# Kernel tuning notes

Measured on AMD Instinct MI355X. Metric: run time of the kernel, lower is better.

## Reference

```python
import jax, jax.numpy as jnp
import numpy as np

# Static config (matches init_kwargs)
T_Q, H_Q, W_Q = 8, 16, 16
T_K, H_K, W_K = 8, 16, 16
HEADS, QDIM = 8, 64


def _rel_dist(q_len, k_len):
    q_ratio = round(max(k_len / q_len, 1.0))
    k_ratio = round(max(q_len / k_len, 1.0))
    d = jnp.arange(q_len)[:, None] * q_ratio - jnp.arange(k_len)[None, :] * k_ratio
    return d + (k_len - 1) * k_ratio  # [q_len, k_len] int indices


def setup_inputs() -> dict:
    key = jax.random.key(0)
    k1, k2, k3, k4, k5 = jax.random.split(key, 5)
    B = 2
    q_tok = T_Q * H_Q * W_Q
    k_tok = T_K * H_K * W_K
    return {
        "query": jax.random.normal(k1, (B, HEADS, q_tok, QDIM), dtype=jnp.float32),
        "scores": jax.random.normal(k2, (B, HEADS, q_tok, k_tok), dtype=jnp.float32),
        "height_emb": jax.random.normal(k3, (2 * (max(H_Q, H_K) - 1) + 1, QDIM), dtype=jnp.float32),
        "width_emb": jax.random.normal(k4, (2 * (max(W_Q, W_K) - 1) + 1, QDIM), dtype=jnp.float32),
        "time_emb": jax.random.normal(k5, (2 * (max(T_Q, T_K) - 1) + 1, QDIM), dtype=jnp.float32),
    }


def reference(query, scores, height_emb, width_emb, time_emb):
    B = query.shape[0]
    # Relative-distance index tables (static)
    dist_h = _rel_dist(H_Q, H_K)  # [H_Q, H_K]
    dist_w = _rel_dist(W_Q, W_K)  # [W_Q, W_K]
    dist_t = _rel_dist(T_Q, T_K)  # [T_Q, T_K]
    Rh = height_emb[dist_h]  # [H_Q, H_K, C]
    Rw = width_emb[dist_w]   # [W_Q, W_K, C]
    Rt = time_emb[dist_t]    # [T_Q, T_K, C]
    q = query.reshape(B, HEADS, T_Q, H_Q, W_Q, QDIM)
    rel_h = jnp.einsum('bNthwc,hkc->bNthwk', q, Rh)  # k = key height
    rel_w = jnp.einsum('bNthwc,wkc->bNthwk', q, Rw)  # k = key width
    rel_t = jnp.einsum('bNthwc,tkc->bNthwk', q, Rt)  # k = key time
    s = scores.reshape(B, HEADS, T_Q, H_Q, W_Q, T_K, H_K, W_K)
    s = (s
         + rel_h[:, :, :, :, :, None, :, None]
         + rel_w[:, :, :, :, :, None, None, :]
         + rel_t[:, :, :, :, :, :, None, None])
    return s.reshape(B, HEADS, T_Q * H_Q * W_Q, T_K * H_K * W_K)
```

## Files before the change

### kernel.cpp

```cpp
#include <hip/hip_runtime.h>

#define T_Q 8
#define H_Q 16
#define W_Q 16
#define HEADS 8
#define QDIM 64
#define QTOK (T_Q * H_Q * W_Q)
#define KTOK 2048

typedef float f32x4 __attribute__((ext_vector_type(4)));

__global__ __launch_bounds__(256)
void relpos_fused_kernel(const float* __restrict__ query,
                         const float* __restrict__ scores,
                         const float* __restrict__ hemb,
                         const float* __restrict__ wemb,
                         const float* __restrict__ temb,
                         float* __restrict__ out)
{
    const int tid  = threadIdx.x;
    const int wid  = tid >> 6;
    const int lane = tid & 63;
    const int row  = blockIdx.x * 4 + wid;
    const int qtok = row & (QTOK - 1);
    const int t = (qtok >> 8) & 7;
    const int h = (qtok >> 4) & 15;
    const int w = qtok & 15;

    __shared__ float q_s[4][QDIM];
    __shared__ float rel[4][40];

    q_s[wid][lane] = __builtin_nontemporal_load(query + (size_t)row * QDIM + lane);
    __syncthreads();

    if (lane < 40) {
        const float* emb;
        if (lane < 16) {
            emb = hemb + (size_t)(h - lane + 15) * QDIM;
        } else if (lane < 32) {
            emb = wemb + (size_t)(w - (lane - 16) + 15) * QDIM;
        } else {
            emb = temb + (size_t)(t - (lane - 32) + 7) * QDIM;
        }
        float acc = 0.f;
        #pragma unroll
        for (int c = 0; c < QDIM; c += 4) {
            f32x4 e  = *reinterpret_cast<const f32x4*>(emb + c);
            f32x4 qv = *reinterpret_cast<const f32x4*>(&q_s[wid][c]);
            acc += qv.x * e.x + qv.y * e.y + qv.z * e.z + qv.w * e.w;
        }
        rel[wid][lane] = acc;
    }
    __syncthreads();

    const float rh  = rel[wid][lane >> 2];
    const int   wk0 = (lane & 3) * 4;
    const float add0 = rh + rel[wid][16 + wk0 + 0];
    const float add1 = rh + rel[wid][16 + wk0 + 1];
    const float add2 = rh + rel[wid][16 + wk0 + 2];
    const float add3 = rh + rel[wid][16 + wk0 + 3];
    float rt[8];
    #pragma unroll
    for (int it = 0; it < 8; ++it) rt[it] = rel[wid][32 + it];

    const size_t base = (size_t)row * KTOK + lane * 4;
    #pragma unroll
    for (int it = 0; it < 8; ++it) {
        const f32x4 s = __builtin_nontemporal_load(
            reinterpret_cast<const f32x4*>(scores + base + it * 256));
        f32x4 o;
        o.x = s.x + add0 + rt[it];
        o.y = s.y + add1 + rt[it];
        o.z = s.z + add2 + rt[it];
        o.w = s.w + add3 + rt[it];
        __builtin_nontemporal_store(o,
            reinterpret_cast<f32x4*>(out + base + it * 256));
    }
}

extern "C" void kernel_launch(void* const* d_in, const int* in_sizes, int n_in,
                              void* d_out, int out_size, void* d_ws, size_t ws_size,
                              hipStream_t stream) {
    const float* query  = (const float*)d_in[0];
    const float* scores = (const float*)d_in[1];
    const float* hemb   = (const float*)d_in[2];
    const float* wemb   = (const float*)d_in[3];
    const float* temb   = (const float*)d_in[4];
    float* out = (float*)d_out;

    const int B = in_sizes[0] / (HEADS * QTOK * QDIM);
    const int rows = B * HEADS * QTOK;

    relpos_fused_kernel<<<rows / 4, 256, 0, stream>>>(query, scores, hemb, wemb, temb, out);
}
```

Before: 100.5 us.

## Prefetch scores before bias compute and process two rows per wave

Each wave now handles two query rows, and all 16 score vectors are loaded into registers before the relative-bias dot products, so the memory latency overlaps the small compute phase and the barriers. The query row is staged into shared memory with global_load_lds, and the dot product uses four independent accumulators. The number of blocks is halved, and register pressure rises from holding 64 floats of scores per thread, which may lower occupancy on a bandwidth-bound kernel.

Measured after the change: 103.1 us. 1.03x slower.

```diff
diff --git a/kernel.cpp b/kernel.cpp
--- a/kernel.cpp
+++ b/kernel.cpp
@@ -21,60 +21,85 @@
     const int tid  = threadIdx.x;
     const int wid  = tid >> 6;
     const int lane = tid & 63;
-    const int row  = blockIdx.x * 4 + wid;
-    const int qtok = row & (QTOK - 1);
-    const int t = (qtok >> 8) & 7;
-    const int h = (qtok >> 4) & 15;
-    const int w = qtok & 15;
+    const int r0   = blockIdx.x * 8 + wid * 2;
+    const int r1   = r0 + 1;
 
-    __shared__ float q_s[4][QDIM];
-    __shared__ float rel[4][40];
+    __shared__ float q_s[8][QDIM];
+    __shared__ float rel[8][40];
 
-    q_s[wid][lane] = __builtin_nontemporal_load(query + (size_t)row * QDIM + lane);
+    const size_t base0 = (size_t)r0 * KTOK + lane * 4;
+    const size_t base1 = (size_t)r1 * KTOK + lane * 4;
+    f32x4 s[16];
+    #pragma unroll
+    for (int it = 0; it < 8; ++it)
+        s[it] = __builtin_nontemporal_load(
+            reinterpret_cast<const f32x4*>(scores + base0 + it * 256));
+    #pragma unroll
+    for (int it = 0; it < 8; ++it)
+        s[8 + it] = __builtin_nontemporal_load(
+            reinterpret_cast<const f32x4*>(scores + base1 + it * 256));
+
+    __builtin_amdgcn_global_load_lds(
+        reinterpret_cast<const unsigned int*>(query + (size_t)r0 * QDIM + lane),
+        reinterpret_cast<unsigned int*>(&q_s[wid * 2][0]), 4, 0, 0);
+    __builtin_amdgcn_global_load_lds(
+        reinterpret_cast<const unsigned int*>(query + (size_t)r1 * QDIM + lane),
+        reinterpret_cast<unsigned int*>(&q_s[wid * 2 + 1][0]), 4, 0, 0);
     __syncthreads();
 
     if (lane < 40) {
-        const float* emb;
-        if (lane < 16) {
-            emb = hemb + (size_t)(h - lane + 15) * QDIM;
-        } else if (lane < 32) {
-            emb = wemb + (size_t)(w - (lane - 16) + 15) * QDIM;
-        } else {
-            emb = temb + (size_t)(t - (lane - 32) + 7) * QDIM;
+        #pragma unroll
+        for (int rr = 0; rr < 2; ++rr) {
+            const int row  = r0 + rr;
+            const int qtok = row & (QTOK - 1);
+            const int t = (qtok >> 8) & 7;
+            const int h = (qtok >> 4) & 15;
+            const int w = qtok & 15;
+            const float* emb;
+            if (lane < 16) {
+                emb = hemb + (size_t)(h - lane + 15) * QDIM;
+            } else if (lane < 32) {
+                emb = wemb + (size_t)(w - (lane - 16) + 15) * QDIM;
+            } else {
+                emb = temb + (size_t)(t - (lane - 32) + 7) * QDIM;
+            }
+            float a0 = 0.f, a1 = 0.f, a2 = 0.f, a3 = 0.f;
+            #pragma unroll
+            for (int c = 0; c < QDIM; c += 4) {
+                f32x4 e  = *reinterpret_cast<const f32x4*>(emb + c);
+                f32x4 qv = *reinterpret_cast<const f32x4*>(&q_s[wid * 2 + rr][c]);
+                a0 += qv.x * e.x;
+                a1 += qv.y * e.y;
+                a2 += qv.z * e.z;
+                a3 += qv.w * e.w;
+            }
+            rel[wid * 2 + rr][lane] = (a0 + a1) + (a2 + a3);
         }
-        float acc = 0.f;
-        #pragma unroll
-        for (int c = 0; c < QDIM; c += 4) {
-            f32x4 e  = *reinterpret_cast<const f32x4*>(emb + c);
-            f32x4 qv = *reinterpret_cast<const f32x4*>(&q_s[wid][c]);
-            acc += qv.x * e.x + qv.y * e.y + qv.z * e.z + qv.w * e.w;
-        }
-        rel[wid][lane] = acc;
     }
     __syncthreads();
 
-    const float rh  = rel[wid][lane >> 2];
-    const int   wk0 = (lane & 3) * 4;
-    const float add0 = rh + rel[wid][16 + wk0 + 0];
-    const float add1 = rh + rel[wid][16 + wk0 + 1];
-    const float add2 = rh + rel[wid][16 + wk0 + 2];
-    const float add3 = rh + rel[wid][16 + wk0 + 3];
-    float rt[8];
+    const int wk0 = (lane & 3) * 4;
     #pragma unroll
-    for (int it = 0; it < 8; ++it) rt[it] = rel[wid][32 + it];
-
-    const size_t base = (size_t)row * KTOK + lane * 4;
-    #pragma unroll
-    for (int it = 0; it < 8; ++it) {
-        const f32x4 s = __builtin_nontemporal_load(
-            reinterpret_cast<const f32x4*>(scores + base + it * 256));
-        f32x4 o;
-        o.x = s.x + add0 + rt[it];
-        o.y = s.y + add1 + rt[it];
-        o.z = s.z + add2 + rt[it];
-        o.w = s.w + add3 + rt[it];
-        __builtin_nontemporal_store(o,
-            reinterpret_cast<f32x4*>(out + base + it * 256));
+    for (int rr = 0; rr < 2; ++rr) {
+        const float* rl = rel[wid * 2 + rr];
+        const float rh   = rl[lane >> 2];
+        const float add0 = rh + rl[16 + wk0 + 0];
+        const float add1 = rh + rl[16 + wk0 + 1];
+        const float add2 = rh + rl[16 + wk0 + 2];
+        const float add3 = rh + rl[16 + wk0 + 3];
+        const size_t base = rr ? base1 : base0;
+        #pragma unroll
+        for (int it = 0; it < 8; ++it) {
+            const float rt = rl[32 + it];
+            const f32x4 sv = s[rr * 8 + it];
+            f32x4 o;
+            o.x = sv.x + add0 + rt;
+            o.y = sv.y + add1 + rt;
+            o.z = sv.z + add2 + rt;
+            o.w = sv.w + add3 + rt;
+            __builtin_nontemporal_store(o,
+                reinterpret_cast<f32x4*>(out + base + it * 256));
+        }
     }
 }
 
@@ -91,5 +116,5 @@
     const int B = in_sizes[0] / (HEADS * QTOK * QDIM);
     const int rows = B * HEADS * QTOK;
 
-    relpos_fused_kernel<<<rows / 4, 256, 0, stream>>>(query, scores, hemb, wemb, temb, out);
+    relpos_fused_kernel<<<rows / 8, 256, 0, stream>>>(query, scores, hemb, wemb, temb, out);
 }
```
